# Kernel tuning notes

Measured on AMD Instinct MI355X. Metric: run time of the kernel, lower is better.

Reference implementation:

```python
import jax, jax.numpy as jnp
import numpy as np

N_NODES = 100000
N_EDGES = 1600000
N_GRAPHS = 512


def _graph_conv(x, W, b, src, dst, n_nodes):
    """DGL GraphConv, norm='both': D_in^-1/2 (A (D_out^-1/2 x)) W + b.
    Weight is applied on the smaller-dim side (same math, less memory)."""
    ones = jnp.ones(src.shape[0], dtype=x.dtype)
    deg_out = jnp.clip(jax.ops.segment_sum(ones, src, num_segments=n_nodes), 1.0)
    deg_in = jnp.clip(jax.ops.segment_sum(ones, dst, num_segments=n_nodes), 1.0)
    h = x * (deg_out ** -0.5)[:, None]
    if W.shape[0] > W.shape[1]:  # reduce feature dim before the SpMM
        h = h @ W
        h = jax.ops.segment_sum(h[src], dst, num_segments=n_nodes)
    else:
        h = jax.ops.segment_sum(h[src], dst, num_segments=n_nodes)
        h = h @ W
    return h * (deg_in ** -0.5)[:, None] + b


def setup_inputs() -> dict:
    key = jax.random.key(0)
    ks = jax.random.split(key, 16)
    x = jax.random.normal(ks[0], (N_NODES, 128), dtype=jnp.float32)
    src = jax.random.randint(ks[1], (N_EDGES,), 0, N_NODES, dtype=jnp.int32)
    dst = jax.random.randint(ks[2], (N_EDGES,), 0, N_NODES, dtype=jnp.int32)
    graph_ids = jnp.sort(jax.random.randint(ks[3], (N_NODES,), 0, N_GRAPHS, dtype=jnp.int32))
    s = 0.05
    return {
        "x": x, "src": src, "dst": dst, "graph_ids": graph_ids,
        "W1": jax.random.normal(ks[4], (128, 256), jnp.float32) * s,
        "b1": jnp.zeros((256,), jnp.float32),
        "W2": jax.random.normal(ks[5], (256, 64), jnp.float32) * s,
        "b2": jnp.zeros((64,), jnp.float32),
        "Wc1": jax.random.normal(ks[6], (64, 18), jnp.float32) * s,
        "bc1": jnp.zeros((18,), jnp.float32),
        "Wc2": jax.random.normal(ks[7], (18, 12), jnp.float32) * s,
        "bc2": jnp.zeros((12,), jnp.float32),
        "Wc3": jax.random.normal(ks[8], (12, 6), jnp.float32) * s,
        "bc3": jnp.zeros((6,), jnp.float32),
        "Wc4": jax.random.normal(ks[9], (6, 2), jnp.float32) * s,
        "bc4": jnp.zeros((2,), jnp.float32),
    }


def reference(x, src, dst, graph_ids, W1, b1, W2, b2, Wc1, bc1, Wc2, bc2, Wc3, bc3, Wc4, bc4):
    n = x.shape[0]
    h = jax.nn.relu(_graph_conv(x, W1, b1, src, dst, n))
    h = jax.nn.relu(_graph_conv(h, W2, b2, src, dst, n))
    # dgl.mean_nodes: per-graph mean over nodes
    sums = jax.ops.segment_sum(h, graph_ids, num_segments=N_GRAPHS)
    cnts = jnp.clip(jax.ops.segment_sum(jnp.ones(n, h.dtype), graph_ids, num_segments=N_GRAPHS), 1.0)
    hg = sums / cnts[:, None]
    # classifier: 4 stacked Linear layers, no activations (faithful to source)
    hg = hg @ Wc1 + bc1
    hg = hg @ Wc2 + bc2
    hg = hg @ Wc3 + bc3
    return hg @ Wc4 + bc4
```

## Files before the change

### kernel.cpp

```cpp
#include <hip/hip_runtime.h>
#include <cstdint>
#include <cstddef>

#define NGRAPHS 512

static inline size_t align_up(size_t x, size_t a){ return (x + a - 1) & ~(a - 1); }

__device__ __forceinline__ unsigned short f2bf(float f){
  unsigned int u = __float_as_uint(f);
  u += 0x7FFFu + ((u >> 16) & 1u);
  return (unsigned short)(u >> 16);
}
__device__ __forceinline__ float bflo(unsigned int u){ return __uint_as_float(u << 16); }
__device__ __forceinline__ float bfhi(unsigned int u){ return __uint_as_float(u & 0xffff0000u); }
__device__ __forceinline__ unsigned int pack2(float a, float b){
  return (unsigned)f2bf(a) | ((unsigned)f2bf(b) << 16);
}

typedef __attribute__((ext_vector_type(8))) short bf16x8;
typedef __attribute__((ext_vector_type(4))) float f32x4;

__global__ __launch_bounds__(256) void k_partcount(const int* __restrict__ src, const int* __restrict__ dst,
                                                   int* __restrict__ cntS, int* __restrict__ cntD, int n_edges, int NBLK,
                                                   const float* __restrict__ W1, unsigned short* __restrict__ Wt1,
                                                   const float* __restrict__ W2, unsigned short* __restrict__ Wt2,
                                                   float* __restrict__ sums,
                                                   const int* __restrict__ gids, int* __restrict__ gb, int n_nodes){
  __shared__ int cs[256], cd[256];
  if (blockIdx.x >= NBLK){
    long long u = (long long)(blockIdx.x - NBLK) * 256 + threadIdx.x;
    if (u < 128 * 256){
      int k = (int)(u / 256), n = (int)(u % 256);
      Wt1[(size_t)n * 128 + k] = f2bf(W1[u]);
      return;
    }
    u -= 128 * 256;
    if (u < 256 * 64){
      int k = (int)(u / 64), n = (int)(u % 64);
      Wt2[(size_t)n * 256 + k] = f2bf(W2[u]);
      return;
    }
    u -= 256 * 64;
    if (u < (long long)NGRAPHS * 64){ sums[u] = 0.f; return; }
    u -= (long long)NGRAPHS * 64;
    if (u < n_nodes){
      int i = (int)u;
      int g  = gids[i];
      int gp = (i > 0) ? gids[i - 1] : -1;
      for (int q = gp + 1; q <= g; ++q) gb[q] = i;
      if (i == n_nodes - 1)
        for (int q = g + 1; q <= NGRAPHS; ++q) gb[q] = n_nodes;
    }
    return;
  }
  int tid = threadIdx.x;
  cs[tid] = 0; cd[tid] = 0;
  __syncthreads();
  int e0 = blockIdx.x * 4096;
  int e1 = min(e0 + 4096, n_edges);
  for (int e = e0 + tid; e < e1; e += 256){
    atomicAdd(&cs[src[e] >> 9], 1);
    atomicAdd(&cd[dst[e] >> 9], 1);
  }
  __syncthreads();
  cntS[blockIdx.x * 256 + tid] = cs[tid];
  cntD[blockIdx.x * 256 + tid] = cd[tid];
}

__global__ __launch_bounds__(256) void k_colscan(int* __restrict__ cntS, int* __restrict__ cntD,
                                                 int* __restrict__ totS, int* __restrict__ totD,
                                                 int nblk, int NB){
  int col = blockIdx.x;
  int* cnt; int* tot; int k;
  if (col < NB){ cnt = cntS; tot = totS; k = col; }
  else         { cnt = cntD; tot = totD; k = col - NB; }
  __shared__ int tsum[256];
  int tid = threadIdx.x;
  int i0 = 2 * tid, i1 = 2 * tid + 1;
  int a = (i0 < nblk) ? cnt[i0 * 256 + k] : 0;
  int b = (i1 < nblk) ? cnt[i1 * 256 + k] : 0;
  int s = a + b;
  tsum[tid] = s;
  __syncthreads();
  for (int off = 1; off < 256; off <<= 1){
    int t = (tid >= off) ? tsum[tid - off] : 0;
    __syncthreads();
    tsum[tid] += t;
    __syncthreads();
  }
  int pre = tsum[tid] - s;
  if (i0 < nblk) cnt[i0 * 256 + k] = pre;
  if (i1 < nblk) cnt[i1 * 256 + k] = pre + a;
  if (tid == 255) tot[k] = tsum[255];
}

__global__ __launch_bounds__(256) void k_scatter_det(const int* __restrict__ src, const int* __restrict__ dst,
                                                     const int* __restrict__ cntS, const int* __restrict__ cntD,
                                                     const int* __restrict__ totS, const int* __restrict__ totD,
                                                     int* __restrict__ baseS, int* __restrict__ baseD,
                                                     int2* __restrict__ pairD, int* __restrict__ srcS,
                                                     int n_edges, int NB){
  __shared__ int s1[256], s2[256], curS[256], curD[256];
  int tid = threadIdx.x;
  int b = blockIdx.x;
  int v1 = (tid < NB) ? totS[tid] : 0;
  int v2 = (tid < NB) ? totD[tid] : 0;
  s1[tid] = v1; s2[tid] = v2;
  __syncthreads();
  for (int off = 1; off < 256; off <<= 1){
    int t1 = (tid >= off) ? s1[tid - off] : 0;
    int t2 = (tid >= off) ? s2[tid - off] : 0;
    __syncthreads();
    s1[tid] += t1; s2[tid] += t2;
    __syncthreads();
  }
  int bS = s1[tid] - v1, bD = s2[tid] - v2;
  if (b == 0 && tid < NB){ baseS[tid] = bS; baseD[tid] = bD; }
  curS[tid] = bS + cntS[b * 256 + tid];
  curD[tid] = bD + cntD[b * 256 + tid];
  __syncthreads();
  int e0 = b * 4096, e1 = min(e0 + 4096, n_edges);
  for (int e = e0 + tid; e < e1; e += 256){
    int s = src[e], d = dst[e];
    int pd = atomicAdd(&curD[d >> 9], 1);
    pairD[pd] = make_int2(s, d);
    int ps = atomicAdd(&curS[s >> 9], 1);
    srcS[ps] = s;
  }
}

__global__ __launch_bounds__(256) void k_bucket_build(const int2* __restrict__ pairD, const int* __restrict__ baseD,
                                                      const int* __restrict__ srcS, const int* __restrict__ baseS,
                                                      int* __restrict__ offs, float* __restrict__ din_s,
                                                      float* __restrict__ dout_s, int* __restrict__ csr_src,
                                                      int NB, int n, int n_edges){
  __shared__ int cd[512], cs[512], cur[512];
  __shared__ int tsum[256];
  int b = blockIdx.x, node0 = b << 9, tid = threadIdx.x;
  int nn = min(512, n - node0);
  for (int i = tid; i < 512; i += 256){ cd[i] = 0; cs[i] = 0; }
  __syncthreads();
  int jd0 = baseD[b], jd1 = (b + 1 < NB) ? baseD[b + 1] : n_edges;
  for (int j = jd0 + tid; j < jd1; j += 256) atomicAdd(&cd[pairD[j].y - node0], 1);
  int js0 = baseS[b], js1 = (b + 1 < NB) ? baseS[b + 1] : n_edges;
  for (int j = js0 + tid; j < js1; j += 256) atomicAdd(&cs[srcS[j] - node0], 1);
  __syncthreads();
  int a0 = cd[2 * tid], a1 = cd[2 * tid + 1];
  int s = a0 + a1;
  tsum[tid] = s;
  __syncthreads();
  for (int off = 1; off < 256; off <<= 1){
    int t = (tid >= off) ? tsum[tid - off] : 0;
    __syncthreads();
    tsum[tid] += t;
    __syncthreads();
  }
  int pre = tsum[tid] - s + jd0;
  cur[2 * tid]     = pre;
  cur[2 * tid + 1] = pre + a0;
  __syncthreads();
  for (int i = tid; i < nn; i += 256){
    offs[node0 + i]   = cur[i];
    din_s[node0 + i]  = 1.0f / sqrtf((float)max(cd[i], 1));
    dout_s[node0 + i] = 1.0f / sqrtf((float)max(cs[i], 1));
  }
  if (b == NB - 1 && tid == 0) offs[n] = n_edges;
  __syncthreads();
  for (int j = jd0 + tid; j < jd1; j += 256){
    int2 e = pairD[j];
    int p = atomicAdd(&cur[e.y - node0], 1);
    csr_src[p] = e.x;
  }
}

__global__ __launch_bounds__(256) void k_prep2(const float* __restrict__ x,
                                               const float* __restrict__ dout_s,
                                               unsigned int* __restrict__ xb, long long total4){
  long long t = (long long)blockIdx.x * 256 + threadIdx.x;
  if (t >= total4) return;
  float4 v = ((const float4*)x)[t];
  float s = dout_s[t >> 5];
  xb[t * 2 + 0] = pack2(v.x * s, v.y * s);
  xb[t * 2 + 1] = pack2(v.z * s, v.w * s);
}

__global__ __launch_bounds__(256) void k_spmm1(const unsigned int* __restrict__ xb,
    const int* __restrict__ offs, const int* __restrict__ csr_src,
    unsigned int* __restrict__ aggb, int n_nodes){
  int node = (blockIdx.x * blockDim.x + threadIdx.x) >> 5;
  int lane = threadIdx.x & 31;
  if (node >= n_nodes) return;
  int j0 = offs[node], j1 = offs[node + 1];
  const uint2* xp = (const uint2*)xb;
  float4 acc = make_float4(0.f, 0.f, 0.f, 0.f);
  int j = j0;
  int nfull = (j1 - j0) >> 3;
  if (nfull > 0){
    int idx[8];
#pragma unroll
    for (int u = 0; u < 8; ++u) idx[u] = csr_src[j + u];
    for (int b = 0; b < nfull; ++b){
      int nidx[8];
      if (b + 1 < nfull){
#pragma unroll
        for (int u = 0; u < 8; ++u) nidx[u] = csr_src[j + 8 + u];
      }
      uint2 v[8];
#pragma unroll
      for (int u = 0; u < 8; ++u) v[u] = xp[(size_t)idx[u] * 32 + lane];
#pragma unroll
      for (int u = 0; u < 8; ++u){
        acc.x += bflo(v[u].x); acc.y += bfhi(v[u].x);
        acc.z += bflo(v[u].y); acc.w += bfhi(v[u].y);
      }
      if (b + 1 < nfull){
#pragma unroll
        for (int u = 0; u < 8; ++u) idx[u] = nidx[u];
      }
      j += 8;
    }
  }
  for (; j < j1; ++j){
    uint2 v = xp[(size_t)csr_src[j] * 32 + lane];
    acc.x += bflo(v.x); acc.y += bfhi(v.x);
    acc.z += bflo(v.y); acc.w += bfhi(v.y);
  }
  uint2 pk;
  pk.x = pack2(acc.x, acc.y);
  pk.y = pack2(acc.z, acc.w);
  ((uint2*)aggb)[(size_t)node * 32 + lane] = pk;
}

__global__ __launch_bounds__(256) void k_gemm1(const unsigned short* __restrict__ A,
    const unsigned short* __restrict__ Bt, unsigned short* __restrict__ C,
    int M, const float* __restrict__ din, const float* __restrict__ dout,
    const float* __restrict__ bias){
  constexpr int LDA = 136;
  __shared__ __align__(16) unsigned short As[128 * LDA];
  __shared__ __align__(16) unsigned short Bs[64 * LDA];
  int tid = threadIdx.x;
  int bm0 = blockIdx.x * 128;
  int wid = tid >> 6, lane = tid & 63;
  int wm = wid * 32;
  int quad = lane >> 4, l16 = lane & 15;

  uint4 areg[8];
#pragma unroll
  for (int it = 0; it < 8; ++it){
    int i = tid + it * 256;
    int m = i >> 4, c = i & 15;
    int gr = bm0 + m;
    areg[it] = (gr < M) ? *(const uint4*)(A + (size_t)gr * 128 + c * 8) : make_uint4(0u, 0u, 0u, 0u);
  }
  uint4 breg[4];
#pragma unroll
  for (int it = 0; it < 4; ++it){
    int i = tid + it * 256;
    int n = i >> 4, c = i & 15;
    breg[it] = *(const uint4*)(Bt + (size_t)n * 128 + c * 8);
  }
#pragma unroll
  for (int it = 0; it < 8; ++it){
    int i = tid + it * 256;
    int m = i >> 4, c = i & 15;
    *(uint4*)&As[m * LDA + c * 8] = areg[it];
  }
#pragma unroll
  for (int it = 0; it < 4; ++it){
    int i = tid + it * 256;
    int n = i >> 4, c = i & 15;
    *(uint4*)&Bs[n * LDA + c * 8] = breg[it];
  }
  float rsv[2][4], rs2v[2][4];
#pragma unroll
  for (int t = 0; t < 2; ++t)
#pragma unroll
    for (int r = 0; r < 4; ++r){
      int gr = bm0 + wm + t * 16 + quad * 4 + r;
      rsv[t][r]  = (gr < M) ? din[gr]  : 0.f;
      rs2v[t][r] = (gr < M) ? dout[gr] : 0.f;
    }
  __syncthreads();

  for (int nt = 0; nt < 4; ++nt){
    if (nt < 3){
#pragma unroll
      for (int it = 0; it < 4; ++it){
        int i = tid + it * 256;
        int n = i >> 4, c = i & 15;
        breg[it] = *(const uint4*)(Bt + (size_t)((nt + 1) * 64 + n) * 128 + c * 8);
      }
    }
    f32x4 acc[2][4];
#pragma unroll
    for (int t = 0; t < 2; ++t)
#pragma unroll
      for (int u = 0; u < 4; ++u) acc[t][u] = f32x4{0.f, 0.f, 0.f, 0.f};
#pragma unroll
    for (int ks = 0; ks < 4; ++ks){
      bf16x8 af[2], bfr[4];
#pragma unroll
      for (int t = 0; t < 2; ++t)
        af[t] = *(const bf16x8*)&As[(wm + t * 16 + l16) * LDA + ks * 32 + quad * 8];
#pragma unroll
      for (int u = 0; u < 4; ++u)
        bfr[u] = *(const bf16x8*)&Bs[(u * 16 + l16) * LDA + ks * 32 + quad * 8];
#pragma unroll
      for (int t = 0; t < 2; ++t)
#pragma unroll
        for (int u = 0; u < 4; ++u)
          acc[t][u] = __builtin_amdgcn_mfma_f32_16x16x32_bf16(af[t], bfr[u], acc[t][u], 0, 0, 0);
    }
    float bv[4];
#pragma unroll
    for (int u = 0; u < 4; ++u) bv[u] = bias[nt * 64 + u * 16 + l16];
#pragma unroll
    for (int t = 0; t < 2; ++t){
#pragma unroll
      for (int r = 0; r < 4; ++r){
        int gr = bm0 + wm + t * 16 + quad * 4 + r;
        if (gr < M){
#pragma unroll
          for (int u = 0; u < 4; ++u){
            float cv = fmaxf(fmaf(acc[t][u][r], rsv[t][r], bv[u]), 0.f) * rs2v[t][r];
            C[(size_t)gr * 256 + nt * 64 + u * 16 + l16] = f2bf(cv);
          }
        }
      }
    }
    if (nt < 3){
      __syncthreads();
#pragma unroll
      for (int it = 0; it < 4; ++it){
        int i = tid + it * 256;
        int n = i >> 4, c = i & 15;
        *(uint4*)&Bs[n * LDA + c * 8] = breg[it];
      }
      __syncthreads();
    }
  }
}

#define SCHUNK 4
__global__ __launch_bounds__(256) void k_spmm2_fused(const unsigned short* __restrict__ t2,
    const int* __restrict__ offs, const int* __restrict__ csr_src,
    const float* __restrict__ din_s, const float* __restrict__ b2,
    const int* __restrict__ gb, float* __restrict__ sums){
  __shared__ float bs[64];
  int tid = threadIdx.x;
  int g = blockIdx.x & (NGRAPHS - 1);
  int chunk = blockIdx.x >> 9;
  int hw = chunk * 8 + (tid >> 5);
  int lane = tid & 31;
  if (tid < 64) bs[tid] = 0.f;
  __syncthreads();
  int g0 = gb[g], g1 = gb[g + 1];
  const unsigned int* tp = (const unsigned int*)t2;
  float2 bb = ((const float2*)b2)[lane];
  float sx = 0.f, sy = 0.f;
  for (int node = g0 + hw; node < g1; node += 32){
    int j0 = offs[node], j1 = offs[node + 1];
    float ax = 0.f, ay = 0.f;
    int j = j0;
    int nfull = (j1 - j0) >> 3;
    if (nfull > 0){
      int idx[8];
#pragma unroll
      for (int u = 0; u < 8; ++u) idx[u] = csr_src[j + u];
      for (int b = 0; b < nfull; ++b){
        int nidx[8];
        if (b + 1 < nfull){
#pragma unroll
          for (int u = 0; u < 8; ++u) nidx[u] = csr_src[j + 8 + u];
        }
        unsigned int v[8];
#pragma unroll
        for (int u = 0; u < 8; ++u) v[u] = tp[(size_t)idx[u] * 32 + lane];
#pragma unroll
        for (int u = 0; u < 8; ++u){ ax += bflo(v[u]); ay += bfhi(v[u]); }
        if (b + 1 < nfull){
#pragma unroll
          for (int u = 0; u < 8; ++u) idx[u] = nidx[u];
        }
        j += 8;
      }
    }
    for (; j < j1; ++j){
      unsigned int v = tp[(size_t)csr_src[j] * 32 + lane];
      ax += bflo(v);
      ay += bfhi(v);
    }
    float ds = din_s[node];
    sx += fmaxf(fmaf(ax, ds, bb.x), 0.f);
    sy += fmaxf(fmaf(ay, ds, bb.y), 0.f);
  }
  atomicAdd(&bs[2 * lane], sx);
  atomicAdd(&bs[2 * lane + 1], sy);
  __syncthreads();
  if (tid < 64) atomicAdd(&sums[(size_t)g * 64 + tid], bs[tid]);
}

template<bool C_BF16, bool EPI, bool EPI2>
__global__ __launch_bounds__(256) void gemm_mfma(
    const unsigned short* __restrict__ A, const unsigned short* __restrict__ Bt, void* __restrict__ Cp,
    int M, int N, int K,
    const float* __restrict__ rowScaleC, const float* __restrict__ rowScaleC2,
    const float* __restrict__ bias){
  constexpr int BM = 128, BN = 64, BK = 32, LDA = 40;
  __shared__ __align__(16) unsigned short As[2][BM * LDA];
  __shared__ __align__(16) unsigned short Bs[2][BN * LDA];
  int tid = threadIdx.x;
  int bm0 = blockIdx.x * BM;
  int bn0 = blockIdx.y * BN;
  int wid = tid >> 6, lane = tid & 63;
  int wm = (wid >> 1) * 64, wn = (wid & 1) * 32;
  int quad = lane >> 4, l16 = lane & 15;
  f32x4 acc[4][2];
#pragma unroll
  for (int t = 0; t < 4; ++t)
#pragma unroll
    for (int u = 0; u < 2; ++u) acc[t][u] = f32x4{0.f, 0.f, 0.f, 0.f};

  uint2 ar[4], br[2];
  auto preload = [&](int kk){
#pragma unroll
    for (int it = 0; it < 4; ++it){
      int i = tid + it * 256;
      int m = i >> 3, c = i & 7;
      int gr = bm0 + m;
      ar[it] = (gr < M) ? *(const uint2*)(A + (size_t)gr * K + kk + c * 4) : make_uint2(0u, 0u);
    }
#pragma unroll
    for (int it = 0; it < 2; ++it){
      int i = tid + it * 256;
      int n = i >> 3, c = i & 7;
      br[it] = *(const uint2*)(Bt + (size_t)(bn0 + n) * K + kk + c * 4);
    }
  };
  auto commit = [&](int buf){
#pragma unroll
    for (int it = 0; it < 4; ++it){
      int i = tid + it * 256;
      int m = i >> 3, c = i & 7;
      *(uint2*)&As[buf][m * LDA + c * 4] = ar[it];
    }
#pragma unroll
    for (int it = 0; it < 2; ++it){
      int i = tid + it * 256;
      int n = i >> 3, c = i & 7;
      *(uint2*)&Bs[buf][n * LDA + c * 4] = br[it];
    }
  };

  preload(0);
  commit(0);
  __syncthreads();
  int nk = K / BK;
  for (int kb = 0; kb < nk; ++kb){
    int cur = kb & 1;
    if (kb + 1 < nk) preload((kb + 1) * BK);
    bf16x8 af[4], bfr[2];
#pragma unroll
    for (int t = 0; t < 4; ++t)
      af[t] = *(const bf16x8*)&As[cur][(wm + t * 16 + l16) * LDA + quad * 8];
#pragma unroll
    for (int u = 0; u < 2; ++u)
      bfr[u] = *(const bf16x8*)&Bs[cur][(wn + u * 16 + l16) * LDA + quad * 8];
#pragma unroll
    for (int t = 0; t < 4; ++t)
#pragma unroll
      for (int u = 0; u < 2; ++u)
        acc[t][u] = __builtin_amdgcn_mfma_f32_16x16x32_bf16(af[t], bfr[u], acc[t][u], 0, 0, 0);
    if (kb + 1 < nk){
      commit(cur ^ 1);
      __syncthreads();
    }
  }
  float bv[2] = {0.f, 0.f};
  if constexpr (EPI){ bv[0] = bias[bn0 + wn + l16]; bv[1] = bias[bn0 + wn + 16 + l16]; }
#pragma unroll
  for (int t = 0; t < 4; ++t){
#pragma unroll
    for (int r = 0; r < 4; ++r){
      int gr = bm0 + wm + t * 16 + quad * 4 + r;
      if (gr < M){
        float rs = 1.f, rs2 = 1.f;
        if constexpr (EPI)  rs  = rowScaleC[gr];
        if constexpr (EPI2) rs2 = rowScaleC2[gr];
#pragma unroll
        for (int u = 0; u < 2; ++u){
          int gc = bn0 + wn + u * 16 + l16;
          float cv = acc[t][u][r];
          if constexpr (EPI)  cv = fmaxf(fmaf(cv, rs, bv[u]), 0.f);
          if constexpr (EPI2) cv *= rs2;
          if constexpr (C_BF16) ((unsigned short*)Cp)[(size_t)gr * N + gc] = f2bf(cv);
          else                  ((float*)Cp)[(size_t)gr * N + gc] = cv;
        }
      }
    }
  }
}

__global__ __launch_bounds__(256) void k_classifier(const float* __restrict__ sums, const int* __restrict__ gb,
    const float* __restrict__ Wc1, const float* __restrict__ bc1,
    const float* __restrict__ Wc2, const float* __restrict__ bc2,
    const float* __restrict__ Wc3, const float* __restrict__ bc3,
    const float* __restrict__ Wc4, const float* __restrict__ bc4,
    float* __restrict__ out){
  __shared__ float w1[64 * 18], w2[18 * 12], w3[12 * 6], w4[6 * 2];
  __shared__ float B1[18], B2[12], B3[6], B4[2];
  int tid = threadIdx.x;
  for (int i = tid; i < 64 * 18; i += 256) w1[i] = Wc1[i];
  for (int i = tid; i < 18 * 12; i += 256) w2[i] = Wc2[i];
  for (int i = tid; i < 12 * 6;  i += 256) w3[i] = Wc3[i];
  for (int i = tid; i < 6 * 2;   i += 256) w4[i] = Wc4[i];
  if (tid < 18) B1[tid] = bc1[tid];
  if (tid < 12) B2[tid] = bc2[tid];
  if (tid < 6)  B3[tid] = bc3[tid];
  if (tid < 2)  B4[tid] = bc4[tid];
  __syncthreads();
  int g = blockIdx.x * 256 + tid;
  float cnt = fmaxf((float)(gb[g + 1] - gb[g]), 1.0f);
  float h[64];
#pragma unroll
  for (int f = 0; f < 64; ++f) h[f] = sums[(size_t)g * 64 + f] / cnt;
  float t1[18];
#pragma unroll
  for (int j = 0; j < 18; ++j){
    float s = B1[j];
    for (int f = 0; f < 64; ++f) s = fmaf(h[f], w1[f * 18 + j], s);
    t1[j] = s;
  }
  float t2[12];
#pragma unroll
  for (int j = 0; j < 12; ++j){
    float s = B2[j];
    for (int f = 0; f < 18; ++f) s = fmaf(t1[f], w2[f * 12 + j], s);
    t2[j] = s;
  }
  float t3[6];
#pragma unroll
  for (int j = 0; j < 6; ++j){
    float s = B3[j];
    for (int f = 0; f < 12; ++f) s = fmaf(t2[f], w3[f * 6 + j], s);
    t3[j] = s;
  }
#pragma unroll
  for (int j = 0; j < 2; ++j){
    float s = B4[j];
    for (int f = 0; f < 6; ++f) s = fmaf(t3[f], w4[f * 2 + j], s);
    out[(size_t)g * 2 + j] = s;
  }
}

extern "C" void kernel_launch(void* const* d_in, const int* in_sizes, int n_in,
                              void* d_out, int out_size, void* d_ws, size_t ws_size,
                              hipStream_t stream){
  const float* x   = (const float*)d_in[0];
  const int*   src = (const int*)d_in[1];
  const int*   dst = (const int*)d_in[2];
  const int*   gid = (const int*)d_in[3];
  const float* W1  = (const float*)d_in[4];
  const float* b1  = (const float*)d_in[5];
  const float* W2  = (const float*)d_in[6];
  const float* b2  = (const float*)d_in[7];
  const float* Wc1 = (const float*)d_in[8];
  const float* bc1 = (const float*)d_in[9];
  const float* Wc2 = (const float*)d_in[10];
  const float* bc2 = (const float*)d_in[11];
  const float* Wc3 = (const float*)d_in[12];
  const float* bc3 = (const float*)d_in[13];
  const float* Wc4 = (const float*)d_in[14];
  const float* bc4 = (const float*)d_in[15];
  float* out = (float*)d_out;

  const int n_nodes = in_sizes[3];
  const int n_edges = in_sizes[1];
  const int F1 = 256, F2 = 64;
  const int NB   = (n_nodes + 511) >> 9;
  const int NBLK = (n_edges + 4095) / 4096;

  char* w = (char*)d_ws;
  size_t o = 0;
  auto alloc = [&](size_t bytes) -> char* {
    char* p = w + o;
    o = align_up(o + bytes, 256);
    return p;
  };
  float* sums      = (float*)alloc((size_t)NGRAPHS * F2 * 4);
  int*   gb        = (int*)  alloc((size_t)(NGRAPHS + 1) * 4);
  int*   cntS      = (int*)  alloc((size_t)NBLK * 256 * 4);
  int*   cntD      = (int*)  alloc((size_t)NBLK * 256 * 4);
  int*   totS      = (int*)  alloc((size_t)256 * 4);
  int*   totD      = (int*)  alloc((size_t)256 * 4);
  int*   baseS     = (int*)  alloc((size_t)256 * 4);
  int*   baseD     = (int*)  alloc((size_t)256 * 4);
  float* dout_s    = (float*)alloc((size_t)n_nodes * 4);
  float* din_s     = (float*)alloc((size_t)n_nodes * 4);
  int*   offs      = (int*)  alloc((size_t)(n_nodes + 1) * 4);
  int*   csr_src   = (int*)  alloc((size_t)n_edges * 4);
  unsigned short* Wt1 = (unsigned short*)alloc((size_t)256 * 128 * 2);
  unsigned short* Wt2 = (unsigned short*)alloc((size_t)64 * 256 * 2);
  unsigned int*   xb  = (unsigned int*)  alloc((size_t)n_nodes * 128 * 2);
  unsigned short* aggb= (unsigned short*)alloc((size_t)n_nodes * 128 * 2);
  unsigned short* h1b = (unsigned short*)alloc((size_t)n_nodes * F1 * 2);
  int2*  pairD = (int2*)aggb;
  int*   srcS  = (int*)((char*)aggb + (size_t)n_edges * 8);
  unsigned short* t2b = aggb;

  {
    long long miscTotal = 128 * 256 + 256 * 64 + (long long)NGRAPHS * 64 + n_nodes;
    int miscBlocks = (int)((miscTotal + 255) / 256);
    k_partcount<<<NBLK + miscBlocks, 256, 0, stream>>>(src, dst, cntS, cntD, n_edges, NBLK,
                                                       W1, Wt1, W2, Wt2, sums, gid, gb, n_nodes);
  }
  k_colscan     <<<2 * NB, 256, 0, stream>>>(cntS, cntD, totS, totD, NBLK, NB);
  k_scatter_det <<<NBLK, 256, 0, stream>>>(src, dst, cntS, cntD, totS, totD, baseS, baseD, pairD, srcS, n_edges, NB);
  k_bucket_build<<<NB, 256, 0, stream>>>(pairD, baseD, srcS, baseS, offs, din_s, dout_s, csr_src, NB, n_nodes, n_edges);

  {
    long long total4 = (long long)n_nodes * 32;
    k_prep2<<<(int)((total4 + 255) / 256), 256, 0, stream>>>(x, dout_s, xb, total4);
  }

  int gx = (n_nodes + 127) / 128;
  {
    long long threads = (long long)n_nodes * 32;
    k_spmm1<<<(int)((threads + 255) / 256), 256, 0, stream>>>(xb, offs, csr_src, (unsigned int*)aggb, n_nodes);
    k_gemm1<<<gx, 256, 0, stream>>>(aggb, Wt1, h1b, n_nodes, din_s, dout_s, b1);
  }
  {
    gemm_mfma<true, false, false><<<dim3(gx, 1), 256, 0, stream>>>(
        h1b, Wt2, t2b, n_nodes, F2, F1, nullptr, nullptr, nullptr);
    k_spmm2_fused<<<NGRAPHS * SCHUNK, 256, 0, stream>>>(t2b, offs, csr_src, din_s, b2, gb, sums);
  }
  k_classifier<<<NGRAPHS / 256, 256, 0, stream>>>(sums, gb, Wc1, bc1, Wc2, bc2, Wc3, bc3, Wc4, bc4, out);
}
```

Baseline: 362.4 us.

## Restructure graph preprocessing and SpMM kernels with global outdeg atomics and LDS-staged scatter

Out-degree is now counted with global atomics, which removes the source-side bucket sort (cntS, colscan and srcS scatter). The dst scatter is staged through LDS so each block writes its bucketed pairs contiguously. The x scaling and bf16 pack is fused into bucket_build, and the zeroing of sums moves to a memset. spmm1 now assigns a 64-lane wave per node with 4-byte loads, and spmm2 splits edges across the two wave halves before a shuffle reduce. The trade-offs are global atomic contention on outdeg and shallower unrolling in the gather loops.

```diff
diff --git a/kernel.cpp b/kernel.cpp
--- a/kernel.cpp
+++ b/kernel.cpp
@@ -21,12 +21,12 @@
 typedef __attribute__((ext_vector_type(4))) float f32x4;
 
 __global__ __launch_bounds__(256) void k_partcount(const int* __restrict__ src, const int* __restrict__ dst,
-                                                   int* __restrict__ cntS, int* __restrict__ cntD, int n_edges, int NBLK,
+                                                   int* __restrict__ cntD, int* __restrict__ outdeg,
+                                                   int n_edges, int NBLK,
                                                    const float* __restrict__ W1, unsigned short* __restrict__ Wt1,
                                                    const float* __restrict__ W2, unsigned short* __restrict__ Wt2,
-                                                   float* __restrict__ sums,
                                                    const int* __restrict__ gids, int* __restrict__ gb, int n_nodes){
-  __shared__ int cs[256], cd[256];
+  __shared__ int cd[256];
   if (blockIdx.x >= NBLK){
     long long u = (long long)(blockIdx.x - NBLK) * 256 + threadIdx.x;
     if (u < 128 * 256){
@@ -41,8 +41,6 @@
       return;
     }
     u -= 256 * 64;
-    if (u < (long long)NGRAPHS * 64){ sums[u] = 0.f; return; }
-    u -= (long long)NGRAPHS * 64;
     if (u < n_nodes){
       int i = (int)u;
       int g  = gids[i];
@@ -54,31 +52,25 @@
     return;
   }
   int tid = threadIdx.x;
-  cs[tid] = 0; cd[tid] = 0;
+  cd[tid] = 0;
   __syncthreads();
   int e0 = blockIdx.x * 4096;
   int e1 = min(e0 + 4096, n_edges);
   for (int e = e0 + tid; e < e1; e += 256){
-    atomicAdd(&cs[src[e] >> 9], 1);
     atomicAdd(&cd[dst[e] >> 9], 1);
-  }
-  __syncthreads();
-  cntS[blockIdx.x * 256 + tid] = cs[tid];
+    atomicAdd(&outdeg[src[e]], 1);
+  }
+  __syncthreads();
   cntD[blockIdx.x * 256 + tid] = cd[tid];
 }
 
-__global__ __launch_bounds__(256) void k_colscan(int* __restrict__ cntS, int* __restrict__ cntD,
-                                                 int* __restrict__ totS, int* __restrict__ totD,
-                                                 int nblk, int NB){
-  int col = blockIdx.x;
-  int* cnt; int* tot; int k;
-  if (col < NB){ cnt = cntS; tot = totS; k = col; }
-  else         { cnt = cntD; tot = totD; k = col - NB; }
+__global__ __launch_bounds__(256) void k_colscan(int* __restrict__ cntD, int* __restrict__ totD, int nblk){
+  int k = blockIdx.x;
   __shared__ int tsum[256];
   int tid = threadIdx.x;
   int i0 = 2 * tid, i1 = 2 * tid + 1;
-  int a = (i0 < nblk) ? cnt[i0 * 256 + k] : 0;
-  int b = (i1 < nblk) ? cnt[i1 * 256 + k] : 0;
+  int a = (i0 < nblk) ? cntD[i0 * 256 + k] : 0;
+  int b = (i1 < nblk) ? cntD[i1 * 256 + k] : 0;
   int s = a + b;
   tsum[tid] = s;
   __syncthreads();
@@ -89,61 +81,80 @@
     __syncthreads();
   }
   int pre = tsum[tid] - s;
-  if (i0 < nblk) cnt[i0 * 256 + k] = pre;
-  if (i1 < nblk) cnt[i1 * 256 + k] = pre + a;
-  if (tid == 255) tot[k] = tsum[255];
+  if (i0 < nblk) cntD[i0 * 256 + k] = pre;
+  if (i1 < nblk) cntD[i1 * 256 + k] = pre + a;
+  if (tid == 255) totD[k] = tsum[255];
 }
 
 __global__ __launch_bounds__(256) void k_scatter_det(const int* __restrict__ src, const int* __restrict__ dst,
-                                                     const int* __restrict__ cntS, const int* __restrict__ cntD,
-                                                     const int* __restrict__ totS, const int* __restrict__ totD,
-                                                     int* __restrict__ baseS, int* __restrict__ baseD,
-                                                     int2* __restrict__ pairD, int* __restrict__ srcS,
+                                                     const int* __restrict__ cntD, const int* __restrict__ totD,
+                                                     int* __restrict__ baseD, int2* __restrict__ pairD,
                                                      int n_edges, int NB){
-  __shared__ int s1[256], s2[256], curS[256], curD[256];
+  __shared__ int s2[256], gbase[256], lscan[256], lcur[256];
+  __shared__ int2 ebuf[4096];
   int tid = threadIdx.x;
   int b = blockIdx.x;
-  int v1 = (tid < NB) ? totS[tid] : 0;
   int v2 = (tid < NB) ? totD[tid] : 0;
-  s1[tid] = v1; s2[tid] = v2;
+  s2[tid] = v2;
   __syncthreads();
   for (int off = 1; off < 256; off <<= 1){
-    int t1 = (tid >= off) ? s1[tid - off] : 0;
     int t2 = (tid >= off) ? s2[tid - off] : 0;
     __syncthreads();
-    s1[tid] += t1; s2[tid] += t2;
-    __syncthreads();
-  }
-  int bS = s1[tid] - v1, bD = s2[tid] - v2;
-  if (b == 0 && tid < NB){ baseS[tid] = bS; baseD[tid] = bD; }
-  curS[tid] = bS + cntS[b * 256 + tid];
-  curD[tid] = bD + cntD[b * 256 + tid];
+    s2[tid] += t2;
+    __syncthreads();
+  }
+  int bD = s2[tid] - v2;
+  if (b == 0 && tid < NB) baseD[tid] = bD;
+  gbase[tid] = bD + cntD[b * 256 + tid];
   __syncthreads();
   int e0 = b * 4096, e1 = min(e0 + 4096, n_edges);
+  int ne = e1 - e0;
+  s2[tid] = 0;
+  __syncthreads();
+  for (int e = e0 + tid; e < e1; e += 256) atomicAdd(&s2[dst[e] >> 9], 1);
+  __syncthreads();
+  int lv = s2[tid];
+  __syncthreads();
+  int sv = lv;
+  s2[tid] = sv;
+  __syncthreads();
+  for (int off = 1; off < 256; off <<= 1){
+    int t2 = (tid >= off) ? s2[tid - off] : 0;
+    __syncthreads();
+    s2[tid] += t2;
+    __syncthreads();
+  }
+  lscan[tid] = s2[tid] - sv;
+  lcur[tid]  = s2[tid] - sv;
+  __syncthreads();
   for (int e = e0 + tid; e < e1; e += 256){
     int s = src[e], d = dst[e];
-    int pd = atomicAdd(&curD[d >> 9], 1);
-    pairD[pd] = make_int2(s, d);
-    int ps = atomicAdd(&curS[s >> 9], 1);
-    srcS[ps] = s;
+    int lp = atomicAdd(&lcur[d >> 9], 1);
+    ebuf[lp] = make_int2(s, d);
+  }
+  __syncthreads();
+  for (int i = tid; i < ne; i += 256){
+    int2 e = ebuf[i];
+    int k = e.y >> 9;
+    pairD[gbase[k] + i - lscan[k]] = e;
   }
 }
 
 __global__ __launch_bounds__(256) void k_bucket_build(const int2* __restrict__ pairD, const int* __restrict__ baseD,
-                                                      const int* __restrict__ srcS, const int* __restrict__ baseS,
+                                                      const int* __restrict__ outdeg,
                                                       int* __restrict__ offs, float* __restrict__ din_s,
                                                       float* __restrict__ dout_s, int* __restrict__ csr_src,
+                                                      const float* __restrict__ x, unsigned int* __restrict__ xb,
                                                       int NB, int n, int n_edges){
-  __shared__ int cd[512], cs[512], cur[512];
+  __shared__ int cd[512], cur[512];
+  __shared__ float sds[512];
   __shared__ int tsum[256];
   int b = blockIdx.x, node0 = b << 9, tid = threadIdx.x;
   int nn = min(512, n - node0);
-  for (int i = tid; i < 512; i += 256){ cd[i] = 0; cs[i] = 0; }
+  for (int i = tid; i < 512; i += 256) cd[i] = 0;
   __syncthreads();
   int jd0 = baseD[b], jd1 = (b + 1 < NB) ? baseD[b + 1] : n_edges;
   for (int j = jd0 + tid; j < jd1; j += 256) atomicAdd(&cd[pairD[j].y - node0], 1);
-  int js0 = baseS[b], js1 = (b + 1 < NB) ? baseS[b + 1] : n_edges;
-  for (int j = js0 + tid; j < js1; j += 256) atomicAdd(&cs[srcS[j] - node0], 1);
   __syncthreads();
   int a0 = cd[2 * tid], a1 = cd[2 * tid + 1];
   int s = a0 + a1;
@@ -162,7 +173,9 @@
   for (int i = tid; i < nn; i += 256){
     offs[node0 + i]   = cur[i];
     din_s[node0 + i]  = 1.0f / sqrtf((float)max(cd[i], 1));
-    dout_s[node0 + i] = 1.0f / sqrtf((float)max(cs[i], 1));
+    float od = 1.0f / sqrtf((float)max(outdeg[node0 + i], 1));
+    dout_s[node0 + i] = od;
+    sds[i] = od;
   }
   if (b == NB - 1 && tid == 0) offs[n] = n_edges;
   __syncthreads();
@@ -171,64 +184,44 @@
     int p = atomicAdd(&cur[e.y - node0], 1);
     csr_src[p] = e.x;
   }
-}
-
-__global__ __launch_bounds__(256) void k_prep2(const float* __restrict__ x,
-                                               const float* __restrict__ dout_s,
-                                               unsigned int* __restrict__ xb, long long total4){
-  long long t = (long long)blockIdx.x * 256 + threadIdx.x;
-  if (t >= total4) return;
-  float4 v = ((const float4*)x)[t];
-  float s = dout_s[t >> 5];
-  xb[t * 2 + 0] = pack2(v.x * s, v.y * s);
-  xb[t * 2 + 1] = pack2(v.z * s, v.w * s);
+  const float4* x4 = (const float4*)x;
+  int tot = nn * 32;
+  for (int i = tid; i < tot; i += 256){
+    float4 v = x4[(size_t)node0 * 32 + i];
+    float sc = sds[i >> 5];
+    size_t o2 = ((size_t)node0 * 32 + i) * 2;
+    xb[o2 + 0] = pack2(v.x * sc, v.y * sc);
+    xb[o2 + 1] = pack2(v.z * sc, v.w * sc);
+  }
 }
 
 __global__ __launch_bounds__(256) void k_spmm1(const unsigned int* __restrict__ xb,
     const int* __restrict__ offs, const int* __restrict__ csr_src,
     unsigned int* __restrict__ aggb, int n_nodes){
-  int node = (blockIdx.x * blockDim.x + threadIdx.x) >> 5;
-  int lane = threadIdx.x & 31;
+  int node = __builtin_amdgcn_readfirstlane((int)((blockIdx.x * 256u + threadIdx.x) >> 6));
   if (node >= n_nodes) return;
+  int lane = threadIdx.x & 63;
   int j0 = offs[node], j1 = offs[node + 1];
-  const uint2* xp = (const uint2*)xb;
-  float4 acc = make_float4(0.f, 0.f, 0.f, 0.f);
+  float ax = 0.f, ay = 0.f;
   int j = j0;
-  int nfull = (j1 - j0) >> 3;
-  if (nfull > 0){
-    int idx[8];
-#pragma unroll
-    for (int u = 0; u < 8; ++u) idx[u] = csr_src[j + u];
-    for (int b = 0; b < nfull; ++b){
-      int nidx[8];
-      if (b + 1 < nfull){
-#pragma unroll
-        for (int u = 0; u < 8; ++u) nidx[u] = csr_src[j + 8 + u];
-      }
-      uint2 v[8];
-#pragma unroll
-      for (int u = 0; u < 8; ++u) v[u] = xp[(size_t)idx[u] * 32 + lane];
-#pragma unroll
-      for (int u = 0; u < 8; ++u){
-        acc.x += bflo(v[u].x); acc.y += bfhi(v[u].x);
-        acc.z += bflo(v[u].y); acc.w += bfhi(v[u].y);
-      }
-      if (b + 1 < nfull){
-#pragma unroll
-        for (int u = 0; u < 8; ++u) idx[u] = nidx[u];
-      }
-      j += 8;
-    }
+  for (; j + 4 <= j1; j += 4){
+    int s0 = csr_src[j + 0];
+    int s1 = csr_src[j + 1];
+    int s2 = csr_src[j + 2];
+    int s3 = csr_src[j + 3];
+    unsigned v0 = xb[(size_t)s0 * 64 + lane];
+    unsigned v1 = xb[(size_t)s1 * 64 + lane];
+    unsigned v2 = xb[(size_t)s2 * 64 + lane];
+    unsigned v3 = xb[(size_t)s3 * 64 + lane];
+    ax += bflo(v0) + bflo(v1) + bflo(v2) + bflo(v3);
+    ay += bfhi(v0) + bfhi(v1) + bfhi(v2) + bfhi(v3);
   }
   for (; j < j1; ++j){
-    uint2 v = xp[(size_t)csr_src[j] * 32 + lane];
-    acc.x += bflo(v.x); acc.y += bfhi(v.x);
-    acc.z += bflo(v.y); acc.w += bfhi(v.y);
-  }
-  uint2 pk;
-  pk.x = pack2(acc.x, acc.y);
-  pk.y = pack2(acc.z, acc.w);
-  ((uint2*)aggb)[(size_t)node * 32 + lane] = pk;
+    unsigned v = xb[(size_t)csr_src[j] * 64 + lane];
+    ax += bflo(v);
+    ay += bfhi(v);
+  }
+  aggb[(size_t)node * 64 + lane] = pack2(ax, ay);
 }
 
 __global__ __launch_bounds__(256) void k_gemm1(const unsigned short* __restrict__ A,
@@ -350,52 +343,40 @@
   int tid = threadIdx.x;
   int g = blockIdx.x & (NGRAPHS - 1);
   int chunk = blockIdx.x >> 9;
-  int hw = chunk * 8 + (tid >> 5);
-  int lane = tid & 31;
+  int wW = __builtin_amdgcn_readfirstlane(chunk * 4 + (tid >> 6));
+  int lane = tid & 63, half = lane >> 5, l = lane & 31;
   if (tid < 64) bs[tid] = 0.f;
   __syncthreads();
   int g0 = gb[g], g1 = gb[g + 1];
   const unsigned int* tp = (const unsigned int*)t2;
-  float2 bb = ((const float2*)b2)[lane];
-  float sx = 0.f, sy = 0.f;
-  for (int node = g0 + hw; node < g1; node += 32){
+  float2 bb = ((const float2*)b2)[l];
+  float gxs = 0.f, gys = 0.f;
+  for (int node = g0 + wW; node < g1; node += 16){
     int j0 = offs[node], j1 = offs[node + 1];
     float ax = 0.f, ay = 0.f;
     int j = j0;
-    int nfull = (j1 - j0) >> 3;
-    if (nfull > 0){
-      int idx[8];
-#pragma unroll
-      for (int u = 0; u < 8; ++u) idx[u] = csr_src[j + u];
-      for (int b = 0; b < nfull; ++b){
-        int nidx[8];
-        if (b + 1 < nfull){
-#pragma unroll
-          for (int u = 0; u < 8; ++u) nidx[u] = csr_src[j + 8 + u];
-        }
-        unsigned int v[8];
-#pragma unroll
-        for (int u = 0; u < 8; ++u) v[u] = tp[(size_t)idx[u] * 32 + lane];
-#pragma unroll
-        for (int u = 0; u < 8; ++u){ ax += bflo(v[u]); ay += bfhi(v[u]); }
-        if (b + 1 < nfull){
-#pragma unroll
-          for (int u = 0; u < 8; ++u) idx[u] = nidx[u];
-        }
-        j += 8;
-      }
-    }
-    for (; j < j1; ++j){
-      unsigned int v = tp[(size_t)csr_src[j] * 32 + lane];
+    for (; j + 2 <= j1; j += 2){
+      int s0 = csr_src[j], s1 = csr_src[j + 1];
+      int ss = half ? s1 : s0;
+      unsigned v = tp[(size_t)ss * 32 + l];
       ax += bflo(v);
       ay += bfhi(v);
     }
+    if (j < j1 && half == 0){
+      unsigned v = tp[(size_t)csr_src[j] * 32 + l];
+      ax += bflo(v);
+      ay += bfhi(v);
+    }
+    ax += __shfl_xor(ax, 32);
+    ay += __shfl_xor(ay, 32);
     float ds = din_s[node];
-    sx += fmaxf(fmaf(ax, ds, bb.x), 0.f);
-    sy += fmaxf(fmaf(ay, ds, bb.y), 0.f);
-  }
-  atomicAdd(&bs[2 * lane], sx);
-  atomicAdd(&bs[2 * lane + 1], sy);
+    gxs += fmaxf(fmaf(ax, ds, bb.x), 0.f);
+    gys += fmaxf(fmaf(ay, ds, bb.y), 0.f);
+  }
+  if (half == 0){
+    atomicAdd(&bs[2 * l], gxs);
+    atomicAdd(&bs[2 * l + 1], gys);
+  }
   __syncthreads();
   if (tid < 64) atomicAdd(&sums[(size_t)g * 64 + tid], bs[tid]);
 }
@@ -588,12 +569,11 @@
     return p;
   };
   float* sums      = (float*)alloc((size_t)NGRAPHS * F2 * 4);
+  int*   outdeg    = (int*)  alloc((size_t)n_nodes * 4);
+  size_t zero_bytes = (size_t)((char*)outdeg + (size_t)n_nodes * 4 - (char*)sums);
   int*   gb        = (int*)  alloc((size_t)(NGRAPHS + 1) * 4);
-  int*   cntS      = (int*)  alloc((size_t)NBLK * 256 * 4);
   int*   cntD      = (int*)  alloc((size_t)NBLK * 256 * 4);
-  int*   totS      = (int*)  alloc((size_t)256 * 4);
   int*   totD      = (int*)  alloc((size_t)256 * 4);
-  int*   baseS     = (int*)  alloc((size_t)256 * 4);
   int*   baseD     = (int*)  alloc((size_t)256 * 4);
   float* dout_s    = (float*)alloc((size_t)n_nodes * 4);
   float* din_s     = (float*)alloc((size_t)n_nodes * 4);
@@ -605,27 +585,24 @@
   unsigned short* aggb= (unsigned short*)alloc((size_t)n_nodes * 128 * 2);
   unsigned short* h1b = (unsigned short*)alloc((size_t)n_nodes * F1 * 2);
   int2*  pairD = (int2*)aggb;
-  int*   srcS  = (int*)((char*)aggb + (size_t)n_edges * 8);
   unsigned short* t2b = aggb;
 
+  hipMemsetAsync(sums, 0, zero_bytes, stream);
+
   {
-    long long miscTotal = 128 * 256 + 256 * 64 + (long long)NGRAPHS * 64 + n_nodes;
+    long long miscTotal = 128 * 256 + 256 * 64 + n_nodes;
     int miscBlocks = (int)((miscTotal + 255) / 256);
-    k_partcount<<<NBLK + miscBlocks, 256, 0, stream>>>(src, dst, cntS, cntD, n_edges, NBLK,
-                                                       W1, Wt1, W2, Wt2, sums, gid, gb, n_nodes);
-  }
-  k_colscan     <<<2 * NB, 256, 0, stream>>>(cntS, cntD, totS, totD, NBLK, NB);
-  k_scatter_det <<<NBLK, 256, 0, stream>>>(src, dst, cntS, cntD, totS, totD, baseS, baseD, pairD, srcS, n_edges, NB);
-  k_bucket_build<<<NB, 256, 0, stream>>>(pairD, baseD, srcS, baseS, offs, din_s, dout_s, csr_src, NB, n_nodes, n_edges);
-
-  {
-    long long total4 = (long long)n_nodes * 32;
-    k_prep2<<<(int)((total4 + 255) / 256), 256, 0, stream>>>(x, dout_s, xb, total4);
-  }
+    k_partcount<<<NBLK + miscBlocks, 256, 0, stream>>>(src, dst, cntD, outdeg, n_edges, NBLK,
+                                                       W1, Wt1, W2, Wt2, gid, gb, n_nodes);
+  }
+  k_colscan     <<<NB, 256, 0, stream>>>(cntD, totD, NBLK);
+  k_scatter_det <<<NBLK, 256, 0, stream>>>(src, dst, cntD, totD, baseD, pairD, n_edges, NB);
+  k_bucket_build<<<NB, 256, 0, stream>>>(pairD, baseD, outdeg, offs, din_s, dout_s, csr_src,
+                                         x, xb, NB, n_nodes, n_edges);
 
   int gx = (n_nodes + 127) / 128;
   {
-    long long threads = (long long)n_nodes * 32;
+    long long threads = (long long)n_nodes * 64;
     k_spmm1<<<(int)((threads + 255) / 256), 256, 0, stream>>>(xb, offs, csr_src, (unsigned int*)aggb, n_nodes);
     k_gemm1<<<gx, 256, 0, stream>>>(aggb, Wt1, h1b, n_nodes, din_s, dout_s, b1);
   }
```

New measurement: 416.7 us. +15.0%, slower.
